# Performance work log

Measured on AMD Instinct MI355X. Metric: run time of the kernel, lower is better.

## Reference

```python
import jax, jax.numpy as jnp
import numpy as np

K = 3      # fixed 3x3 kernel in module
PAD = 1    # padding=1, stride=1, dilation=1, groups=1, deformable_groups=1


def _conv2d(x, w, b=None, pad=PAD):
    out = jax.lax.conv_general_dilated(
        x, w, window_strides=(1, 1), padding=((pad, pad), (pad, pad)),
        dimension_numbers=('NCHW', 'OIHW', 'NCHW'))
    if b is not None:
        out = out + b[None, :, None, None]
    return out


def _bilinear_gather(x, py, px):
    # x: [B,C,H,W]; py,px: [B,KK,H,W] float sampling coords (zero-pad outside)
    B, C, H, W = x.shape
    y0 = jnp.floor(py)
    x0 = jnp.floor(px)
    wy1 = py - y0
    wx1 = px - x0
    wy0 = 1.0 - wy1
    wx0 = 1.0 - wx1
    y0i = y0.astype(jnp.int32)
    x0i = x0.astype(jnp.int32)
    xf = x.reshape(B, C, H * W)

    def corner(yi, xi, w):
        valid = (yi >= 0) & (yi < H) & (xi >= 0) & (xi < W)
        yc = jnp.clip(yi, 0, H - 1)
        xc = jnp.clip(xi, 0, W - 1)
        idx = (yc * W + xc).reshape(B, -1)                     # [B, KK*H*W]
        v = jnp.take_along_axis(xf, idx[:, None, :], axis=2)  # [B, C, KK*H*W]
        return v * (w * valid).reshape(B, 1, -1)

    out = (corner(y0i,     x0i,     wy0 * wx0)
         + corner(y0i,     x0i + 1, wy0 * wx1)
         + corner(y0i + 1, x0i,     wy1 * wx0)
         + corner(y0i + 1, x0i + 1, wy1 * wx1))
    KK = py.shape[1]
    return out.reshape(B, C, KK, H, W)


def _deform_forward(x, offset_w, offset_b, conv_w):
    B, C, H, W = x.shape
    # offset branch: plain 3x3 conv -> [B, 2*K*K, H, W], layout (k, (dy,dx))
    off = _conv2d(x, offset_w, offset_b).reshape(B, K * K, 2, H, W)
    ys = jnp.arange(H, dtype=x.dtype)
    xs = jnp.arange(W, dtype=x.dtype)
    ky, kx = jnp.meshgrid(jnp.arange(K), jnp.arange(K), indexing='ij')
    ky = ky.reshape(-1).astype(x.dtype)   # [9]
    kx = kx.reshape(-1).astype(x.dtype)
    # sampling coords p = p0 + p_k + offset   -> [B, 9, H, W]
    py = ys[None, None, :, None] - PAD + ky[None, :, None, None] + off[:, :, 0]
    px = xs[None, None, None, :] - PAD + kx[None, :, None, None] + off[:, :, 1]
    sampled = _bilinear_gather(x, py, px)                       # [B,C,9,H,W]
    O = conv_w.shape[0]
    return jnp.einsum('bckhw,ock->bohw', sampled, conv_w.reshape(O, C, K * K))


def setup_inputs() -> dict:
    key = jax.random.key(0)
    k1, k2, k3 = jax.random.split(key, 3)
    B, C, O, H, W = 8, 256, 256, 64, 64
    x = jax.random.normal(k1, (B, C, H, W), dtype=jnp.float32)
    # small random offset weights so learned offsets are ~ +/- 2 px
    offset_w = jax.random.normal(k2, (2 * K * K, C, K, K), dtype=jnp.float32) * 0.05
    offset_b = jnp.zeros((2 * K * K,), dtype=jnp.float32)
    conv_w = jax.random.normal(k3, (O, C, K, K), dtype=jnp.float32) * 0.02
    return {"x": x, "offset_w": offset_w, "offset_b": offset_b, "conv_w": conv_w}


def reference(x, offset_w, offset_b, conv_w):
    return _deform_forward(x, offset_w, offset_b, conv_w)
```

## Files before the change

kernel.cpp:

```cpp
#include <hip/hip_runtime.h>

using short8 = __attribute__((ext_vector_type(8))) short;
using f32x4  = __attribute__((ext_vector_type(4))) float;

__device__ inline unsigned short f2bf(float f) {
  unsigned u = __float_as_uint(f);
  u += 0x7fffu + ((u >> 16) & 1u);
  return (unsigned short)(u >> 16);
}
__device__ inline float bf2f(short s) {
  return __uint_as_float(((unsigned)(unsigned short)s) << 16);
}

__device__ inline void barrier_lgkm() {
  asm volatile("s_waitcnt lgkmcnt(0)\n\ts_barrier" ::: "memory");
}

__global__ __launch_bounds__(256) void prep_all(
    const float* __restrict__ x, const float* __restrict__ cw,
    const float* __restrict__ ow, unsigned short* __restrict__ xT,
    unsigned short* __restrict__ xTlo, unsigned short* __restrict__ wBt2,
    unsigned short* __restrict__ wOt, unsigned short* __restrict__ wOtLo) {
  __shared__ float tile[32 * 268];
  int bid = blockIdx.x, tid = threadIdx.x;
  if (bid < 1024) {
    int xh = bid & 1, y = (bid >> 1) & 63, b = bid >> 7;
    int xc = tid & 31, cq = tid >> 5;
#pragma unroll 4
    for (int i = 0; i < 32; ++i) {
      int c = i * 8 + cq;
      tile[xc * 268 + c] =
          x[(((size_t)((b << 8) + c)) << 12) + (y << 6) + xh * 32 + xc];
    }
    __syncthreads();
#pragma unroll 2
    for (int i = 0; i < 8; ++i) {
      int u = i * 256 + tid;
      int site = u >> 6, c4 = u & 63;
      float4 v = *(const float4*)(tile + site * 268 + c4 * 4);
      ushort4 hi, lo;
      hi.x = f2bf(v.x); lo.x = f2bf(v.x - bf2f(hi.x));
      hi.y = f2bf(v.y); lo.y = f2bf(v.y - bf2f(hi.y));
      hi.z = f2bf(v.z); lo.z = f2bf(v.z - bf2f(hi.z));
      hi.w = f2bf(v.w); lo.w = f2bf(v.w - bf2f(hi.w));
      size_t addr = (((size_t)((b << 12) + (y << 6) + xh * 32 + site)) << 8) + c4 * 4;
      *(ushort4*)(xT + addr) = hi;
      *(ushort4*)(xTlo + addr) = lo;
    }
  } else if (bid < 3328) {
    int e = (bid - 1024) * 256 + tid;
    int kc = e & 31, o = (e >> 5) & 255, ks = e >> 13;
    int c = (ks & 7) * 32 + kc, kt = ks >> 3;
    wBt2[e] = f2bf(cw[(size_t)(o * 256 + c) * 9 + kt]);
  } else {
    int e = (bid - 3328) * 256 + tid;
    int kc = e & 31, o = (e >> 5) & 31, ks = e >> 10;
    int c = (ks & 7) * 32 + kc, kt = ks >> 3;
    float v = (o < 18) ? ow[(size_t)(o * 256 + c) * 9 + kt] : 0.f;
    unsigned short hi = f2bf(v);
    wOt[e] = hi;
    wOtLo[e] = f2bf(v - bf2f(hi));
  }
}

__device__ inline void gatherOff2(const unsigned short* xT, const unsigned short* xTlo,
                                  const unsigned short* zp, int b, int h, int p16,
                                  int q, int ccg, int ky, int kx,
                                  short8* gh, short8* gl) {
  int y = h + ky - 1;
  bool yv = (unsigned)y < 64u;
  int yc = min(max(y, 0), 63);
#pragma unroll
  for (int i = 0; i < 4; ++i) {
    int px = i * 16 + p16;
    int xx = px + kx - 1;
    bool v = yv && ((unsigned)xx < 64u);
    int xc = min(max(xx, 0), 63);
    size_t base = (((size_t)((b << 12) + (yc << 6) + xc)) << 8) + ccg * 32 + q * 8;
    const unsigned short* ph = v ? (xT + base) : zp;
    const unsigned short* pl = v ? (xTlo + base) : zp;
    gh[i] = *(const short8*)ph;
    gl[i] = *(const short8*)pl;
  }
}
__device__ inline void loadBOff2(const unsigned short* wOt, const unsigned short* wOtLo,
                                 int ks, int m16, int quad, short8* bh, short8* bl) {
  const unsigned short* bp = wOt + (ks << 10) + m16 * 32 + quad * 8;
  const unsigned short* bq = wOtLo + (ks << 10) + m16 * 32 + quad * 8;
  bh[0] = *(const short8*)bp;  bh[1] = *(const short8*)(bp + 512);
  bl[0] = *(const short8*)bq;  bl[1] = *(const short8*)(bq + 512);
}

__global__ __launch_bounds__(64) void offset_conv3(
    const unsigned short* __restrict__ xT, const unsigned short* __restrict__ xTlo,
    const unsigned short* __restrict__ wOt, const unsigned short* __restrict__ wOtLo,
    const unsigned short* __restrict__ zp, float* out) {
  __shared__ unsigned short Ah[2 * 2560], Al[2 * 2560];
  int lane = threadIdx.x;
  int bid = blockIdx.x;
  int b = bid & 7, h = (bid >> 3) & 63, ccq = bid >> 9;
  int m16 = lane & 15, quad = lane >> 4;
  int p16 = lane >> 2, q = lane & 3;
  f32x4 acc[4][2];
#pragma unroll
  for (int mt = 0; mt < 4; ++mt)
#pragma unroll
    for (int j = 0; j < 2; ++j) acc[mt][j] = (f32x4){0.f, 0.f, 0.f, 0.f};

  short8 gh[4], gl[4], bh[2], bl[2];
  gatherOff2(xT, xTlo, zp, b, h, p16, q, ccq, 0, 0, gh, gl);
  loadBOff2(wOt, wOtLo, ccq, m16, quad, bh, bl);

  for (int it = 0; it < 9; ++it) {
    int buf = it & 1;
#pragma unroll
    for (int i = 0; i < 4; ++i) {
      int px = i * 16 + p16;
      *(short8*)(Ah + buf * 2560 + px * 40 + q * 8) = gh[i];
      *(short8*)(Al + buf * 2560 + px * 40 + q * 8) = gl[i];
    }
    int jn = (it < 8) ? it + 1 : 8;
    int kyn = jn / 3, kxn = jn - kyn * 3;
    short8 ghn[4], gln[4], bhn[2], bln[2];
    loadBOff2(wOt, wOtLo, jn * 8 + ccq, m16, quad, bhn, bln);
    gatherOff2(xT, xTlo, zp, b, h, p16, q, ccq, kyn, kxn, ghn, gln);
#pragma unroll
    for (int mt = 0; mt < 4; ++mt) {
      short8 ah = *(const short8*)(Ah + buf * 2560 + (mt * 16 + m16) * 40 + quad * 8);
      short8 al = *(const short8*)(Al + buf * 2560 + (mt * 16 + m16) * 40 + quad * 8);
#pragma unroll
      for (int j = 0; j < 2; ++j) {
        acc[mt][j] = __builtin_amdgcn_mfma_f32_16x16x32_bf16(ah, bh[j], acc[mt][j], 0, 0, 0);
        acc[mt][j] = __builtin_amdgcn_mfma_f32_16x16x32_bf16(al, bh[j], acc[mt][j], 0, 0, 0);
        acc[mt][j] = __builtin_amdgcn_mfma_f32_16x16x32_bf16(ah, bl[j], acc[mt][j], 0, 0, 0);
      }
    }
#pragma unroll
    for (int i = 0; i < 4; ++i) { gh[i] = ghn[i]; gl[i] = gln[i]; }
    bh[0] = bhn[0]; bh[1] = bhn[1]; bl[0] = bln[0]; bl[1] = bln[1];
  }
#pragma unroll
  for (int j = 0; j < 2; ++j) {
    int o = j * 16 + m16;
    if (o < 18) {
      float* po = out + (((size_t)((b << 8) + 100 + ccq * 18 + o)) << 12) + (h << 6);
#pragma unroll
      for (int mt = 0; mt < 4; ++mt)
#pragma unroll
        for (int rr = 0; rr < 4; ++rr)
          po[mt * 16 + quad * 4 + rr] = acc[mt][j][rr];
    }
  }
}

__device__ inline void gather4(const unsigned short* __restrict__ xT,
                               int bbase, int q, int jt,
                               const int2* cif2, const float4* cwf4,
                               int px, short8* g, float4& wq) {
  int cc = jt / 9, kt = jt - cc * 9;
  int2 si = cif2[kt * 64 + px];
  wq = cwf4[kt * 64 + px];
  const unsigned short* base = xT + (size_t)(unsigned)(bbase + cc * 32 + q * 8);
  g[0] = *(const short8*)(base + si.x);
  g[1] = *(const short8*)(base + si.x + 256);
  g[2] = *(const short8*)(base + si.y);
  g[3] = *(const short8*)(base + si.y + 256);
}
__device__ inline void loadB(const unsigned short* __restrict__ wBt2, int wave,
                             int m16, int quad, int jt, short8* bf) {
  int cc = jt / 9, kt = jt - cc * 9;
  int ks = kt * 8 + cc;
  const unsigned short* bp =
      wBt2 + ((size_t)ks << 13) + (wave << 11) + m16 * 32 + quad * 8;
#pragma unroll
  for (int j = 0; j < 4; ++j)
    bf[j] = *(const short8*)(bp + j * 512);
}

__global__ __launch_bounds__(256, 2) void deform_main(
    const unsigned short* __restrict__ xT, const float* __restrict__ offb,
    const unsigned short* __restrict__ wBt2, float* out) {
  __shared__ float4 smem4[1504];
  char* smem = (char*)smem4;
  float4* cwf4 = (float4*)smem;
  int2*   cif2 = (int2*)(smem + 9216);
  unsigned short* At = (unsigned short*)(smem + 13824);

  int tid = threadIdx.x, lane = tid & 63, wave = tid >> 6;
  int b = blockIdx.x & 7, h = blockIdx.x >> 3;

  size_t bb = ((size_t)(b << 8)) << 12;
  for (int it = tid; it < 576; it += 256) {
    int k = it >> 6, px = it & 63;
    int ky = k / 3, kx = k - ky * 3;
    int idx = (h << 6) + px;
    float dy = offb[2 * k], dx = offb[2 * k + 1];
#pragma unroll
    for (int qq = 0; qq < 8; ++qq) {
      dy += out[bb + (((size_t)(100 + qq * 18 + 2 * k)) << 12) + idx];
      dx += out[bb + (((size_t)(101 + qq * 18 + 2 * k)) << 12) + idx];
    }
    float py = (float)(h - 1 + ky) + dy;
    float pxx = (float)(px - 1 + kx) + dx;
    float y0f = floorf(py), x0f = floorf(pxx);
    int y0 = (int)y0f, x0 = (int)x0f;
    float wy1 = py - y0f, wx1 = pxx - x0f;
    int xb; float wxl, wxr;
    if (x0 >= 0 && x0 <= 62)      { xb = x0; wxl = 1.f - wx1; wxr = wx1; }
    else if (x0 == -1)            { xb = 0;  wxl = wx1;       wxr = 0.f; }
    else if (x0 == 63)            { xb = 62; wxl = 0.f;       wxr = 1.f - wx1; }
    else                          { xb = 0;  wxl = 0.f;       wxr = 0.f; }
    float wy0v = ((unsigned)y0 < 64u) ? (1.f - wy1) : 0.f;
    float wy1v = ((unsigned)(y0 + 1) < 64u) ? wy1 : 0.f;
    int yc0 = min(max(y0, 0), 63), yc1 = min(max(y0 + 1, 0), 63);
    cwf4[it] = make_float4(wy0v * wxl, wy0v * wxr, wy1v * wxl, wy1v * wxr);
    cif2[it] = make_int2(((yc0 << 6) + xb) << 8, ((yc1 << 6) + xb) << 8);
  }
  __syncthreads();

  int m16 = lane & 15, quad = lane >> 4;
  int px = wave * 16 + (lane >> 2);
  int q  = lane & 3;
  int bbase = b << 20;
  f32x4 acc[4][4];
#pragma unroll
  for (int i = 0; i < 4; ++i)
#pragma unroll
    for (int j = 0; j < 4; ++j) acc[i][j] = (f32x4){0.f, 0.f, 0.f, 0.f};

  short8 g[4]; float4 wq; short8 bcur[4];
  gather4(xT, bbase, q, 0, cif2, cwf4, px, g, wq);
  loadB(wBt2, wave, m16, quad, 0, bcur);

  for (int it = 0; it < 72; ++it) {
    int buf = it & 1;
    short8 av;
#pragma unroll
    for (int i = 0; i < 8; ++i) {
      float v = wq.x * bf2f(g[0][i]) + wq.y * bf2f(g[1][i]) +
                wq.z * bf2f(g[2][i]) + wq.w * bf2f(g[3][i]);
      av[i] = (short)f2bf(v);
    }
    *(short8*)(At + buf * 2560 + px * 40 + q * 8) = av;
    int jn = (it < 71) ? it + 1 : 71;
    short8 bnext[4], gn[4]; float4 wqn;
    loadB(wBt2, wave, m16, quad, jn, bnext);
    gather4(xT, bbase, q, jn, cif2, cwf4, px, gn, wqn);
    barrier_lgkm();
    short8 af[4];
#pragma unroll
    for (int mt = 0; mt < 4; ++mt)
      af[mt] = *(const short8*)(At + buf * 2560 + (mt * 16 + m16) * 40 + quad * 8);
#pragma unroll
    for (int mt = 0; mt < 4; ++mt)
#pragma unroll
      for (int j = 0; j < 4; ++j)
        acc[mt][j] = __builtin_amdgcn_mfma_f32_16x16x32_bf16(af[mt], bcur[j],
                                                             acc[mt][j], 0, 0, 0);
#pragma unroll
    for (int i = 0; i < 4; ++i) g[i] = gn[i];
    wq = wqn;
#pragma unroll
    for (int j = 0; j < 4; ++j) bcur[j] = bnext[j];
  }

#pragma unroll
  for (int j = 0; j < 4; ++j) {
    int o = wave * 64 + j * 16 + m16;
    float* po = out + (((size_t)((b << 8) + o)) << 12) + (h << 6) + quad * 4;
#pragma unroll
    for (int mt = 0; mt < 4; ++mt) {
      float4 v = make_float4(acc[mt][j][0], acc[mt][j][1], acc[mt][j][2],
                             acc[mt][j][3]);
      *(float4*)(po + mt * 16) = v;
    }
  }
}

extern "C" void kernel_launch(void* const* d_in, const int* in_sizes, int n_in,
                              void* d_out, int out_size, void* d_ws, size_t ws_size,
                              hipStream_t stream) {
  const float* x     = (const float*)d_in[0];
  const float* offw  = (const float*)d_in[1];
  const float* offb  = (const float*)d_in[2];
  const float* convw = (const float*)d_in[3];
  float* out = (float*)d_out;

  char* ws = (char*)d_ws;
  unsigned short* wOt   = (unsigned short*)ws;
  unsigned short* wOtLo = (unsigned short*)(ws + 147456);
  unsigned short* wBt2  = (unsigned short*)(ws + 294912);
  unsigned short* xT    = (unsigned short*)(ws + 1474560);
  unsigned short* xTlo  = (unsigned short*)(ws + 18251776);
  const unsigned short* zp = wOt + 768;

  prep_all<<<3616, 256, 0, stream>>>(x, convw, offw, xT, xTlo, wBt2, wOt, wOtLo);
  offset_conv3<<<4096, 64, 0, stream>>>(xT, xTlo, wOt, wOtLo, zp, out);
  deform_main<<<512, 256, 0, stream>>>(xT, offb, wBt2, out);
}
```

Baseline: 185.5 us.

## Split deform_main K loop across two wave groups with LDS reduction

deform_main now launches 512 threads per block. The two groups of four waves each handle half of the 72 K-steps in separate LDS buffers, and their partial accumulators are summed through shared memory before kernel group 0 writes the output. This doubles resident waves per CU to hide gather and global-load latency, since the grid has only 512 blocks. The cost is an extra LDS reduction with barriers and a tighter register budget from launch_bounds(512,4). Separately, offset_conv3 drops LDS double buffering because its single-wave block does not need it.

```diff
diff --git a/kernel.cpp b/kernel.cpp
--- a/kernel.cpp
+++ b/kernel.cpp
@@ -95,7 +95,7 @@
     const unsigned short* __restrict__ xT, const unsigned short* __restrict__ xTlo,
     const unsigned short* __restrict__ wOt, const unsigned short* __restrict__ wOtLo,
     const unsigned short* __restrict__ zp, float* out) {
-  __shared__ unsigned short Ah[2 * 2560], Al[2 * 2560];
+  __shared__ unsigned short Ah[2560], Al[2560];
   int lane = threadIdx.x;
   int bid = blockIdx.x;
   int b = bid & 7, h = (bid >> 3) & 63, ccq = bid >> 9;
@@ -112,12 +112,11 @@
   loadBOff2(wOt, wOtLo, ccq, m16, quad, bh, bl);
 
   for (int it = 0; it < 9; ++it) {
-    int buf = it & 1;
 #pragma unroll
     for (int i = 0; i < 4; ++i) {
       int px = i * 16 + p16;
-      *(short8*)(Ah + buf * 2560 + px * 40 + q * 8) = gh[i];
-      *(short8*)(Al + buf * 2560 + px * 40 + q * 8) = gl[i];
+      *(short8*)(Ah + px * 40 + q * 8) = gh[i];
+      *(short8*)(Al + px * 40 + q * 8) = gl[i];
     }
     int jn = (it < 8) ? it + 1 : 8;
     int kyn = jn / 3, kxn = jn - kyn * 3;
@@ -126,8 +125,8 @@
     gatherOff2(xT, xTlo, zp, b, h, p16, q, ccq, kyn, kxn, ghn, gln);
 #pragma unroll
     for (int mt = 0; mt < 4; ++mt) {
-      short8 ah = *(const short8*)(Ah + buf * 2560 + (mt * 16 + m16) * 40 + quad * 8);
-      short8 al = *(const short8*)(Al + buf * 2560 + (mt * 16 + m16) * 40 + quad * 8);
+      short8 ah = *(const short8*)(Ah + (mt * 16 + m16) * 40 + quad * 8);
+      short8 al = *(const short8*)(Al + (mt * 16 + m16) * 40 + quad * 8);
 #pragma unroll
       for (int j = 0; j < 2; ++j) {
         acc[mt][j] = __builtin_amdgcn_mfma_f32_16x16x32_bf16(ah, bh[j], acc[mt][j], 0, 0, 0);
@@ -166,31 +165,32 @@
   g[2] = *(const short8*)(base + si.y);
   g[3] = *(const short8*)(base + si.y + 256);
 }
-__device__ inline void loadB(const unsigned short* __restrict__ wBt2, int wave,
+__device__ inline void loadB(const unsigned short* __restrict__ wBt2, int wv,
                              int m16, int quad, int jt, short8* bf) {
   int cc = jt / 9, kt = jt - cc * 9;
   int ks = kt * 8 + cc;
   const unsigned short* bp =
-      wBt2 + ((size_t)ks << 13) + (wave << 11) + m16 * 32 + quad * 8;
+      wBt2 + ((size_t)ks << 13) + (wv << 11) + m16 * 32 + quad * 8;
 #pragma unroll
   for (int j = 0; j < 4; ++j)
     bf[j] = *(const short8*)(bp + j * 512);
 }
 
-__global__ __launch_bounds__(256, 2) void deform_main(
+__global__ __launch_bounds__(512, 4) void deform_main(
     const unsigned short* __restrict__ xT, const float* __restrict__ offb,
     const unsigned short* __restrict__ wBt2, float* out) {
-  __shared__ float4 smem4[1504];
+  __shared__ float4 smem4[2144];
   char* smem = (char*)smem4;
   float4* cwf4 = (float4*)smem;
   int2*   cif2 = (int2*)(smem + 9216);
   unsigned short* At = (unsigned short*)(smem + 13824);
 
   int tid = threadIdx.x, lane = tid & 63, wave = tid >> 6;
+  int kg = wave >> 2, wv = wave & 3;
   int b = blockIdx.x & 7, h = blockIdx.x >> 3;
 
   size_t bb = ((size_t)(b << 8)) << 12;
-  for (int it = tid; it < 576; it += 256) {
+  for (int it = tid; it < 576; it += 512) {
     int k = it >> 6, px = it & 63;
     int ky = k / 3, kx = k - ky * 3;
     int idx = (h << 6) + px;
@@ -219,7 +219,7 @@
   __syncthreads();
 
   int m16 = lane & 15, quad = lane >> 4;
-  int px = wave * 16 + (lane >> 2);
+  int px = wv * 16 + (lane >> 2);
   int q  = lane & 3;
   int bbase = b << 20;
   f32x4 acc[4][4];
@@ -228,11 +228,14 @@
 #pragma unroll
     for (int j = 0; j < 4; ++j) acc[i][j] = (f32x4){0.f, 0.f, 0.f, 0.f};
 
+  unsigned short* Abase = At + kg * 5120;
+  const int jt0 = kg * 36;
+
   short8 g[4]; float4 wq; short8 bcur[4];
-  gather4(xT, bbase, q, 0, cif2, cwf4, px, g, wq);
-  loadB(wBt2, wave, m16, quad, 0, bcur);
-
-  for (int it = 0; it < 72; ++it) {
+  gather4(xT, bbase, q, jt0, cif2, cwf4, px, g, wq);
+  loadB(wBt2, wv, m16, quad, jt0, bcur);
+
+  for (int it = 0; it < 36; ++it) {
     int buf = it & 1;
     short8 av;
 #pragma unroll
@@ -241,16 +244,16 @@
                 wq.z * bf2f(g[2][i]) + wq.w * bf2f(g[3][i]);
       av[i] = (short)f2bf(v);
     }
-    *(short8*)(At + buf * 2560 + px * 40 + q * 8) = av;
-    int jn = (it < 71) ? it + 1 : 71;
+    *(short8*)(Abase + buf * 2560 + px * 40 + q * 8) = av;
+    int jn = jt0 + ((it < 35) ? it + 1 : 35);
     short8 bnext[4], gn[4]; float4 wqn;
-    loadB(wBt2, wave, m16, quad, jn, bnext);
+    loadB(wBt2, wv, m16, quad, jn, bnext);
     gather4(xT, bbase, q, jn, cif2, cwf4, px, gn, wqn);
     barrier_lgkm();
     short8 af[4];
 #pragma unroll
     for (int mt = 0; mt < 4; ++mt)
-      af[mt] = *(const short8*)(At + buf * 2560 + (mt * 16 + m16) * 40 + quad * 8);
+      af[mt] = *(const short8*)(Abase + buf * 2560 + (mt * 16 + m16) * 40 + quad * 8);
 #pragma unroll
     for (int mt = 0; mt < 4; ++mt)
 #pragma unroll
@@ -264,15 +267,38 @@
     for (int j = 0; j < 4; ++j) bcur[j] = bnext[j];
   }
 
+  __syncthreads();
+  f32x4* red = (f32x4*)smem;
 #pragma unroll
   for (int j = 0; j < 4; ++j) {
-    int o = wave * 64 + j * 16 + m16;
-    float* po = out + (((size_t)((b << 8) + o)) << 12) + (h << 6) + quad * 4;
-#pragma unroll
-    for (int mt = 0; mt < 4; ++mt) {
-      float4 v = make_float4(acc[mt][j][0], acc[mt][j][1], acc[mt][j][2],
-                             acc[mt][j][3]);
-      *(float4*)(po + mt * 16) = v;
+    if (kg == 1) {
+#pragma unroll
+      for (int mt = 0; mt < 4; ++mt)
+        red[(mt * 4 + wv) * 64 + lane] = acc[mt][j];
+    }
+    __syncthreads();
+    if (kg == 0) {
+#pragma unroll
+      for (int mt = 0; mt < 4; ++mt) {
+        f32x4 v = red[(mt * 4 + wv) * 64 + lane];
+        acc[mt][j][0] += v[0]; acc[mt][j][1] += v[1];
+        acc[mt][j][2] += v[2]; acc[mt][j][3] += v[3];
+      }
+    }
+    __syncthreads();
+  }
+
+  if (kg == 0) {
+#pragma unroll
+    for (int j = 0; j < 4; ++j) {
+      int o = wv * 64 + j * 16 + m16;
+      float* po = out + (((size_t)((b << 8) + o)) << 12) + (h << 6) + quad * 4;
+#pragma unroll
+      for (int mt = 0; mt < 4; ++mt) {
+        float4 v = make_float4(acc[mt][j][0], acc[mt][j][1], acc[mt][j][2],
+                               acc[mt][j][3]);
+        *(float4*)(po + mt * 16) = v;
+      }
     }
   }
 }
@@ -296,5 +322,5 @@
 
   prep_all<<<3616, 256, 0, stream>>>(x, convw, offw, xT, xTlo, wBt2, wOt, wOtLo);
   offset_conv3<<<4096, 64, 0, stream>>>(xT, xTlo, wOt, wOtLo, zp, out);
-  deform_main<<<512, 256, 0, stream>>>(xT, offb, wBt2, out);
-}
+  deform_main<<<512, 512, 0, stream>>>(xT, offb, wBt2, out);
+}
```

After: 265.5 us. +43.2%, slower.

## Split deform_main rows into half-row blocks, run four blocks per CU

Applied to the files above, without the earlier changes.

deform_main now gives each block half an image row (32 pixels), so it launches twice as many blocks. Shared memory and the accumulator count are halved, which allows launch bounds of four blocks per CU. Only two of the four waves gather and blend the samples, and the conv weights are loaded each iteration instead of being prefetched one step ahead. In exchange, weight reuse per block is halved and weight-load latency is no longer hidden, while the higher occupancy is meant to hide it instead. offset_conv3 also drops its double-buffered LDS staging, relying on in-order LDS access within its single wave.

```diff
diff --git a/kernel.cpp b/kernel.cpp
--- a/kernel.cpp
+++ b/kernel.cpp
@@ -95,7 +95,7 @@
     const unsigned short* __restrict__ xT, const unsigned short* __restrict__ xTlo,
     const unsigned short* __restrict__ wOt, const unsigned short* __restrict__ wOtLo,
     const unsigned short* __restrict__ zp, float* out) {
-  __shared__ unsigned short Ah[2 * 2560], Al[2 * 2560];
+  __shared__ unsigned short Ah[2560], Al[2560];
   int lane = threadIdx.x;
   int bid = blockIdx.x;
   int b = bid & 7, h = (bid >> 3) & 63, ccq = bid >> 9;
@@ -112,12 +112,11 @@
   loadBOff2(wOt, wOtLo, ccq, m16, quad, bh, bl);
 
   for (int it = 0; it < 9; ++it) {
-    int buf = it & 1;
 #pragma unroll
     for (int i = 0; i < 4; ++i) {
       int px = i * 16 + p16;
-      *(short8*)(Ah + buf * 2560 + px * 40 + q * 8) = gh[i];
-      *(short8*)(Al + buf * 2560 + px * 40 + q * 8) = gl[i];
+      *(short8*)(Ah + px * 40 + q * 8) = gh[i];
+      *(short8*)(Al + px * 40 + q * 8) = gl[i];
     }
     int jn = (it < 8) ? it + 1 : 8;
     int kyn = jn / 3, kxn = jn - kyn * 3;
@@ -126,8 +125,8 @@
     gatherOff2(xT, xTlo, zp, b, h, p16, q, ccq, kyn, kxn, ghn, gln);
 #pragma unroll
     for (int mt = 0; mt < 4; ++mt) {
-      short8 ah = *(const short8*)(Ah + buf * 2560 + (mt * 16 + m16) * 40 + quad * 8);
-      short8 al = *(const short8*)(Al + buf * 2560 + (mt * 16 + m16) * 40 + quad * 8);
+      short8 ah = *(const short8*)(Ah + (mt * 16 + m16) * 40 + quad * 8);
+      short8 al = *(const short8*)(Al + (mt * 16 + m16) * 40 + quad * 8);
 #pragma unroll
       for (int j = 0; j < 2; ++j) {
         acc[mt][j] = __builtin_amdgcn_mfma_f32_16x16x32_bf16(ah, bh[j], acc[mt][j], 0, 0, 0);
@@ -156,10 +155,10 @@
 __device__ inline void gather4(const unsigned short* __restrict__ xT,
                                int bbase, int q, int jt,
                                const int2* cif2, const float4* cwf4,
-                               int px, short8* g, float4& wq) {
+                               int lpx, short8* g, float4& wq) {
   int cc = jt / 9, kt = jt - cc * 9;
-  int2 si = cif2[kt * 64 + px];
-  wq = cwf4[kt * 64 + px];
+  int2 si = cif2[kt * 32 + lpx];
+  wq = cwf4[kt * 32 + lpx];
   const unsigned short* base = xT + (size_t)(unsigned)(bbase + cc * 32 + q * 8);
   g[0] = *(const short8*)(base + si.x);
   g[1] = *(const short8*)(base + si.x + 256);
@@ -177,21 +176,23 @@
     bf[j] = *(const short8*)(bp + j * 512);
 }
 
-__global__ __launch_bounds__(256, 2) void deform_main(
+__global__ __launch_bounds__(256, 4) void deform_main(
     const unsigned short* __restrict__ xT, const float* __restrict__ offb,
     const unsigned short* __restrict__ wBt2, float* out) {
-  __shared__ float4 smem4[1504];
+  __shared__ float4 smem4[752];
   char* smem = (char*)smem4;
   float4* cwf4 = (float4*)smem;
-  int2*   cif2 = (int2*)(smem + 9216);
-  unsigned short* At = (unsigned short*)(smem + 13824);
+  int2*   cif2 = (int2*)(smem + 4608);
+  unsigned short* At = (unsigned short*)(smem + 6912);
 
   int tid = threadIdx.x, lane = tid & 63, wave = tid >> 6;
-  int b = blockIdx.x & 7, h = blockIdx.x >> 3;
+  int bid = blockIdx.x;
+  int mh = bid & 1, b = (bid >> 1) & 7, h = bid >> 4;
 
   size_t bb = ((size_t)(b << 8)) << 12;
-  for (int it = tid; it < 576; it += 256) {
-    int k = it >> 6, px = it & 63;
+  for (int it = tid; it < 288; it += 256) {
+    int k = it >> 5, lpx = it & 31;
+    int px = mh * 32 + lpx;
     int ky = k / 3, kx = k - ky * 3;
     int idx = (h << 6) + px;
     float dy = offb[2 * k], dx = offb[2 * k + 1];
@@ -219,57 +220,60 @@
   __syncthreads();
 
   int m16 = lane & 15, quad = lane >> 4;
-  int px = wave * 16 + (lane >> 2);
-  int q  = lane & 3;
+  int lpx = (wave & 1) * 16 + (lane >> 2);
+  int q   = lane & 3;
+  bool stager = (wave < 2);
   int bbase = b << 20;
-  f32x4 acc[4][4];
-#pragma unroll
-  for (int i = 0; i < 4; ++i)
+  f32x4 acc[2][4];
+#pragma unroll
+  for (int i = 0; i < 2; ++i)
 #pragma unroll
     for (int j = 0; j < 4; ++j) acc[i][j] = (f32x4){0.f, 0.f, 0.f, 0.f};
 
-  short8 g[4]; float4 wq; short8 bcur[4];
-  gather4(xT, bbase, q, 0, cif2, cwf4, px, g, wq);
-  loadB(wBt2, wave, m16, quad, 0, bcur);
+  short8 g[4]; float4 wq;
+  if (stager) gather4(xT, bbase, q, 0, cif2, cwf4, lpx, g, wq);
 
   for (int it = 0; it < 72; ++it) {
     int buf = it & 1;
-    short8 av;
-#pragma unroll
-    for (int i = 0; i < 8; ++i) {
-      float v = wq.x * bf2f(g[0][i]) + wq.y * bf2f(g[1][i]) +
-                wq.z * bf2f(g[2][i]) + wq.w * bf2f(g[3][i]);
-      av[i] = (short)f2bf(v);
-    }
-    *(short8*)(At + buf * 2560 + px * 40 + q * 8) = av;
-    int jn = (it < 71) ? it + 1 : 71;
-    short8 bnext[4], gn[4]; float4 wqn;
-    loadB(wBt2, wave, m16, quad, jn, bnext);
-    gather4(xT, bbase, q, jn, cif2, cwf4, px, gn, wqn);
+    short8 gn[4]; float4 wqn;
+    if (stager) {
+      short8 av;
+#pragma unroll
+      for (int i = 0; i < 8; ++i) {
+        float v = wq.x * bf2f(g[0][i]) + wq.y * bf2f(g[1][i]) +
+                  wq.z * bf2f(g[2][i]) + wq.w * bf2f(g[3][i]);
+        av[i] = (short)f2bf(v);
+      }
+      *(short8*)(At + buf * 1280 + lpx * 40 + q * 8) = av;
+      int jn = (it < 71) ? it + 1 : 71;
+      gather4(xT, bbase, q, jn, cif2, cwf4, lpx, gn, wqn);
+    }
+    short8 bcur[4];
+    loadB(wBt2, wave, m16, quad, it, bcur);
     barrier_lgkm();
-    short8 af[4];
-#pragma unroll
-    for (int mt = 0; mt < 4; ++mt)
-      af[mt] = *(const short8*)(At + buf * 2560 + (mt * 16 + m16) * 40 + quad * 8);
-#pragma unroll
-    for (int mt = 0; mt < 4; ++mt)
+    short8 af[2];
+#pragma unroll
+    for (int mt = 0; mt < 2; ++mt)
+      af[mt] = *(const short8*)(At + buf * 1280 + (mt * 16 + m16) * 40 + quad * 8);
+#pragma unroll
+    for (int mt = 0; mt < 2; ++mt)
 #pragma unroll
       for (int j = 0; j < 4; ++j)
         acc[mt][j] = __builtin_amdgcn_mfma_f32_16x16x32_bf16(af[mt], bcur[j],
                                                              acc[mt][j], 0, 0, 0);
-#pragma unroll
-    for (int i = 0; i < 4; ++i) g[i] = gn[i];
-    wq = wqn;
-#pragma unroll
-    for (int j = 0; j < 4; ++j) bcur[j] = bnext[j];
+    if (stager) {
+#pragma unroll
+      for (int i = 0; i < 4; ++i) g[i] = gn[i];
+      wq = wqn;
+    }
   }
 
 #pragma unroll
   for (int j = 0; j < 4; ++j) {
     int o = wave * 64 + j * 16 + m16;
-    float* po = out + (((size_t)((b << 8) + o)) << 12) + (h << 6) + quad * 4;
-#pragma unroll
-    for (int mt = 0; mt < 4; ++mt) {
+    float* po = out + (((size_t)((b << 8) + o)) << 12) + (h << 6) + mh * 32 + quad * 4;
+#pragma unroll
+    for (int mt = 0; mt < 2; ++mt) {
       float4 v = make_float4(acc[mt][j][0], acc[mt][j][1], acc[mt][j][2],
                              acc[mt][j][3]);
       *(float4*)(po + mt * 16) = v;
@@ -296,5 +300,5 @@
 
   prep_all<<<3616, 256, 0, stream>>>(x, convw, offw, xT, xTlo, wBt2, wOt, wOtLo);
   offset_conv3<<<4096, 64, 0, stream>>>(xT, xTlo, wOt, wOtLo, zp, out);
-  deform_main<<<512, 256, 0, stream>>>(xT, offb, wBt2, out);
-}
+  deform_main<<<1024, 256, 0, stream>>>(xT, offb, wBt2, out);
+}
```

Measured after the change: 212.1 us. +14.4%, slower.

## Process two output rows per deform block to share weight fragments

Applied to the files above, without the earlier changes.

The main deformable kernel now launches 512-thread blocks that each cover two image rows. Its eight waves form a 2x4 grid over rows and output-channel groups, so each loaded weight fragment serves twice as many pixels, which halves weight-load traffic per output. Sampling tables and the A tile in shared memory double in size, and the grid halves to 256 blocks, one wave of blocks across the device. Separately, the offset conv kernel drops its double-buffered LDS staging to a single buffer, since it runs as one wave.

```diff
diff --git a/kernel.cpp b/kernel.cpp
--- a/kernel.cpp
+++ b/kernel.cpp
@@ -95,7 +95,7 @@
     const unsigned short* __restrict__ xT, const unsigned short* __restrict__ xTlo,
     const unsigned short* __restrict__ wOt, const unsigned short* __restrict__ wOtLo,
     const unsigned short* __restrict__ zp, float* out) {
-  __shared__ unsigned short Ah[2 * 2560], Al[2 * 2560];
+  __shared__ unsigned short Ah[2560], Al[2560];
   int lane = threadIdx.x;
   int bid = blockIdx.x;
   int b = bid & 7, h = (bid >> 3) & 63, ccq = bid >> 9;
@@ -112,12 +112,11 @@
   loadBOff2(wOt, wOtLo, ccq, m16, quad, bh, bl);
 
   for (int it = 0; it < 9; ++it) {
-    int buf = it & 1;
 #pragma unroll
     for (int i = 0; i < 4; ++i) {
       int px = i * 16 + p16;
-      *(short8*)(Ah + buf * 2560 + px * 40 + q * 8) = gh[i];
-      *(short8*)(Al + buf * 2560 + px * 40 + q * 8) = gl[i];
+      *(short8*)(Ah + px * 40 + q * 8) = gh[i];
+      *(short8*)(Al + px * 40 + q * 8) = gl[i];
     }
     int jn = (it < 8) ? it + 1 : 8;
     int kyn = jn / 3, kxn = jn - kyn * 3;
@@ -126,8 +125,8 @@
     gatherOff2(xT, xTlo, zp, b, h, p16, q, ccq, kyn, kxn, ghn, gln);
 #pragma unroll
     for (int mt = 0; mt < 4; ++mt) {
-      short8 ah = *(const short8*)(Ah + buf * 2560 + (mt * 16 + m16) * 40 + quad * 8);
-      short8 al = *(const short8*)(Al + buf * 2560 + (mt * 16 + m16) * 40 + quad * 8);
+      short8 ah = *(const short8*)(Ah + (mt * 16 + m16) * 40 + quad * 8);
+      short8 al = *(const short8*)(Al + (mt * 16 + m16) * 40 + quad * 8);
 #pragma unroll
       for (int j = 0; j < 2; ++j) {
         acc[mt][j] = __builtin_amdgcn_mfma_f32_16x16x32_bf16(ah, bh[j], acc[mt][j], 0, 0, 0);
@@ -156,42 +155,46 @@
 __device__ inline void gather4(const unsigned short* __restrict__ xT,
                                int bbase, int q, int jt,
                                const int2* cif2, const float4* cwf4,
-                               int px, short8* g, float4& wq) {
+                               int lpx, short8* g, float4& wq) {
   int cc = jt / 9, kt = jt - cc * 9;
-  int2 si = cif2[kt * 64 + px];
-  wq = cwf4[kt * 64 + px];
+  int2 si = cif2[kt * 128 + lpx];
+  wq = cwf4[kt * 128 + lpx];
   const unsigned short* base = xT + (size_t)(unsigned)(bbase + cc * 32 + q * 8);
   g[0] = *(const short8*)(base + si.x);
   g[1] = *(const short8*)(base + si.x + 256);
   g[2] = *(const short8*)(base + si.y);
   g[3] = *(const short8*)(base + si.y + 256);
 }
-__device__ inline void loadB(const unsigned short* __restrict__ wBt2, int wave,
+__device__ inline void loadB(const unsigned short* __restrict__ wBt2, int wc,
                              int m16, int quad, int jt, short8* bf) {
   int cc = jt / 9, kt = jt - cc * 9;
   int ks = kt * 8 + cc;
   const unsigned short* bp =
-      wBt2 + ((size_t)ks << 13) + (wave << 11) + m16 * 32 + quad * 8;
+      wBt2 + ((size_t)ks << 13) + (wc << 11) + m16 * 32 + quad * 8;
 #pragma unroll
   for (int j = 0; j < 4; ++j)
     bf[j] = *(const short8*)(bp + j * 512);
 }
 
-__global__ __launch_bounds__(256, 2) void deform_main(
+__global__ __launch_bounds__(512, 2) void deform_main(
     const unsigned short* __restrict__ xT, const float* __restrict__ offb,
     const unsigned short* __restrict__ wBt2, float* out) {
-  __shared__ float4 smem4[1504];
+  __shared__ float4 smem4[3008];
   char* smem = (char*)smem4;
   float4* cwf4 = (float4*)smem;
-  int2*   cif2 = (int2*)(smem + 9216);
-  unsigned short* At = (unsigned short*)(smem + 13824);
+  int2*   cif2 = (int2*)(smem + 18432);
+  unsigned short* At = (unsigned short*)(smem + 27648);
 
   int tid = threadIdx.x, lane = tid & 63, wave = tid >> 6;
-  int b = blockIdx.x & 7, h = blockIdx.x >> 3;
+  int bid = blockIdx.x;
+  int b = bid & 7, h2 = bid >> 3;
+  int wr = wave >> 2, wc = wave & 3;
 
   size_t bb = ((size_t)(b << 8)) << 12;
-  for (int it = tid; it < 576; it += 256) {
-    int k = it >> 6, px = it & 63;
+  for (int it = tid; it < 1152; it += 512) {
+    int k = it >> 7, px128 = it & 127;
+    int hrow = px128 >> 6, px = px128 & 63;
+    int h = h2 * 2 + hrow;
     int ky = k / 3, kx = k - ky * 3;
     int idx = (h << 6) + px;
     float dy = offb[2 * k], dx = offb[2 * k + 1];
@@ -219,8 +222,8 @@
   __syncthreads();
 
   int m16 = lane & 15, quad = lane >> 4;
-  int px = wave * 16 + (lane >> 2);
-  int q  = lane & 3;
+  int lpx = wave * 16 + (lane >> 2);
+  int q   = lane & 3;
   int bbase = b << 20;
   f32x4 acc[4][4];
 #pragma unroll
@@ -229,8 +232,8 @@
     for (int j = 0; j < 4; ++j) acc[i][j] = (f32x4){0.f, 0.f, 0.f, 0.f};
 
   short8 g[4]; float4 wq; short8 bcur[4];
-  gather4(xT, bbase, q, 0, cif2, cwf4, px, g, wq);
-  loadB(wBt2, wave, m16, quad, 0, bcur);
+  gather4(xT, bbase, q, 0, cif2, cwf4, lpx, g, wq);
+  loadB(wBt2, wc, m16, quad, 0, bcur);
 
   for (int it = 0; it < 72; ++it) {
     int buf = it & 1;
@@ -241,16 +244,17 @@
                 wq.z * bf2f(g[2][i]) + wq.w * bf2f(g[3][i]);
       av[i] = (short)f2bf(v);
     }
-    *(short8*)(At + buf * 2560 + px * 40 + q * 8) = av;
+    *(short8*)(At + buf * 5120 + lpx * 40 + q * 8) = av;
     int jn = (it < 71) ? it + 1 : 71;
     short8 bnext[4], gn[4]; float4 wqn;
-    loadB(wBt2, wave, m16, quad, jn, bnext);
-    gather4(xT, bbase, q, jn, cif2, cwf4, px, gn, wqn);
+    loadB(wBt2, wc, m16, quad, jn, bnext);
+    gather4(xT, bbase, q, jn, cif2, cwf4, lpx, gn, wqn);
     barrier_lgkm();
     short8 af[4];
 #pragma unroll
     for (int mt = 0; mt < 4; ++mt)
-      af[mt] = *(const short8*)(At + buf * 2560 + (mt * 16 + m16) * 40 + quad * 8);
+      af[mt] = *(const short8*)(At + buf * 5120 +
+                                (wr * 64 + mt * 16 + m16) * 40 + quad * 8);
 #pragma unroll
     for (int mt = 0; mt < 4; ++mt)
 #pragma unroll
@@ -266,8 +270,9 @@
 
 #pragma unroll
   for (int j = 0; j < 4; ++j) {
-    int o = wave * 64 + j * 16 + m16;
-    float* po = out + (((size_t)((b << 8) + o)) << 12) + (h << 6) + quad * 4;
+    int o = wc * 64 + j * 16 + m16;
+    float* po = out + (((size_t)((b << 8) + o)) << 12) +
+                ((h2 * 2 + wr) << 6) + quad * 4;
 #pragma unroll
     for (int mt = 0; mt < 4; ++mt) {
       float4 v = make_float4(acc[mt][j][0], acc[mt][j][1], acc[mt][j][2],
@@ -296,5 +301,5 @@
 
   prep_all<<<3616, 256, 0, stream>>>(x, convw, offw, xT, xTlo, wBt2, wOt, wOtLo);
   offset_conv3<<<4096, 64, 0, stream>>>(xT, xTlo, wOt, wOtLo, zp, out);
-  deform_main<<<512, 256, 0, stream>>>(xT, offb, wBt2, out);
-}
+  deform_main<<<256, 512, 0, stream>>>(xT, offb, wBt2, out);
+}
```

Result: slower. 197.0 us (+6.2%).
